# Optimization experiments

Hardware: AMD Instinct MI355X
Metric: run time of the kernel (lower is better)

The kernel has to match this reference:

```python
import jax, jax.numpy as jnp
import numpy as np
from jax.scipy.special import erf

B, S, D, H, F = 2, 2048, 1024, 16, 4096
EPS = 1e-5


def setup_inputs() -> dict:
    key = jax.random.key(0)
    ks = jax.random.split(key, 7)
    s = 0.02  # init scale so attention logits stay in a sane range
    return {
        "x": jax.random.normal(ks[0], (B, S, D), jnp.float32),
        "wq": jax.random.normal(ks[1], (D, D), jnp.float32) * s,
        "wk": jax.random.normal(ks[2], (D, D), jnp.float32) * s,
        "wv": jax.random.normal(ks[3], (D, D), jnp.float32) * s,
        "wo": jax.random.normal(ks[4], (D, D), jnp.float32) * s,
        "w1": jax.random.normal(ks[5], (F, D), jnp.float32) * s,
        "w2": jax.random.normal(ks[6], (D, F), jnp.float32) * s,
        "g1": jnp.ones((D,), jnp.float32),
        "g2": jnp.ones((D,), jnp.float32),
    }


def _rmsnorm(x, g):
    return x / jnp.sqrt(jnp.mean(x * x, axis=-1, keepdims=True) + EPS) * g


def _gelu_exact(x):
    # 0.5 * x * (1 + erf(x / sqrt(2)))
    return 0.5 * x * (1.0 + erf(x * (1.0 / np.sqrt(2.0).astype(np.float32))))


def reference(x, wq, wk, wv, wo, w1, w2, g1, g2):
    b, s, d = x.shape
    dk = d // H
    # --- attention sublayer (pre-RMSNorm) ---
    h = _rmsnorm(x, g1)
    # Linear(bias=False): y = h @ W.T; split heads -> [b, H, s, dk]
    q = (h @ wq.T).reshape(b, s, H, dk).transpose(0, 2, 1, 3)
    k = (h @ wk.T).reshape(b, s, H, dk).transpose(0, 2, 1, 3)
    v = (h @ wv.T).reshape(b, s, H, dk).transpose(0, 2, 1, 3)
    scores = jnp.einsum('bhqd,bhkd->bhqk', q, k) / jnp.sqrt(jnp.float32(dk))
    causal = jnp.triu(jnp.ones((s, s), bool), 1)  # True above diagonal -> masked
    scores = jnp.where(causal, -jnp.inf, scores)
    attn = jax.nn.softmax(scores, axis=-1)
    o = jnp.einsum('bhqk,bhkd->bhqd', attn, v)
    o = o.transpose(0, 2, 1, 3).reshape(b, s, d) @ wo.T
    x = x + o
    # --- FFN sublayer (pre-RMSNorm, exact-erf GELU) ---
    h2 = _rmsnorm(x, g2)
    f = _gelu_exact(h2 @ w1.T) @ w2.T
    return x + f
```

## Files before the change

### kernel.cpp

```cpp
#include <hip/hip_runtime.h>
#include <hip/hip_bf16.h>
#include <math.h>

#define B_   2
#define S_   2048
#define D_   1024
#define H_   16
#define DK_  64
#define F_   4096
#define NTOK (B_ * S_)

typedef __bf16 bf16x8 __attribute__((ext_vector_type(8)));
typedef float  f32x4  __attribute__((ext_vector_type(4)));

__device__ __forceinline__ unsigned short bf16r(float f) {
  unsigned u = __builtin_bit_cast(unsigned, f);
  u += 0x7fffu + ((u >> 16) & 1u);
  return (unsigned short)(u >> 16);
}

__device__ __forceinline__ void gload_lds16(const void* g, void* l) {
  __builtin_amdgcn_global_load_lds(
      (__attribute__((address_space(1))) void*)g,
      (__attribute__((address_space(3))) void*)l, 16, 0, 0);
}

__device__ __forceinline__ unsigned lds_off(void* p) {
  return (unsigned)(size_t)(__attribute__((address_space(3))) void*)p;
}
__device__ __forceinline__ bf16x8 ds_read16(unsigned a) {
  bf16x8 r;
  asm volatile("ds_read_b128 %0, %1" : "=v"(r) : "v"(a));
  return r;
}
__device__ __forceinline__ void ds_write32(unsigned a, unsigned v) {
  asm volatile("ds_write_b32 %0, %1" : : "v"(a), "v"(v));
}
__device__ __forceinline__ void ds_write16b(unsigned a, unsigned v) {
  asm volatile("ds_write_b16 %0, %1" : : "v"(a), "v"(v));
}
__device__ __forceinline__ float fexp2(float x) {
  float r;
  asm volatile("v_exp_f32 %0, %1\n\ts_nop 0" : "=v"(r) : "v"(x));
  return r;
}
__device__ __forceinline__ unsigned cvt_pk_bf16(float lo, float hi) {
  unsigned r;
  asm volatile("v_cvt_pk_bf16_f32 %0, %1, %2" : "=v"(r) : "v"(lo), "v"(hi));
  return r;
}

__device__ __forceinline__ float gelu_fast(float x) {
  float y = 0.7978845608f * x * (1.0f + 0.044715f * x * x);
  float e = fexp2(2.885390082f * y);
  float t = 1.0f - 2.0f / (e + 1.0f);
  return 0.5f * x * (1.0f + t);
}

#define QSCL 0.18033688f

struct CvtArgs {
  const float* src[6];
  unsigned short* dst[6];
  int start[7];
};
__global__ __launch_bounds__(256) void cvt_all_kernel(CvtArgs a) {
  int i = blockIdx.x * blockDim.x + threadIdx.x;
  if (i >= a.start[6]) return;
  int k = 0;
#pragma unroll
  for (int j = 1; j < 6; ++j)
    if (i >= a.start[j]) k = j;
  int off = i - a.start[k];
  float4 v = reinterpret_cast<const float4*>(a.src[k])[off];
  ushort4 o;
  o.x = bf16r(v.x); o.y = bf16r(v.y); o.z = bf16r(v.z); o.w = bf16r(v.w);
  reinterpret_cast<ushort4*>(a.dst[k])[off] = o;
}

__global__ __launch_bounds__(256) void rmsnorm_kernel(
    const float* __restrict__ x, const float* __restrict__ g,
    unsigned short* __restrict__ out) {
  int row = blockIdx.x;
  int t = threadIdx.x, lane = t & 63, w = t >> 6;
  float4 v = reinterpret_cast<const float4*>(x + (size_t)row * D_)[t];
  float ss = v.x * v.x + v.y * v.y + v.z * v.z + v.w * v.w;
#pragma unroll
  for (int d = 1; d < 64; d <<= 1) ss += __shfl_xor(ss, d);
  __shared__ float red[4];
  if (lane == 0) red[w] = ss;
  __syncthreads();
  float tot = red[0] + red[1] + red[2] + red[3];
  float rstd = rsqrtf(tot * (1.0f / D_) + 1e-5f);
  float4 gv = reinterpret_cast<const float4*>(g)[t];
  ushort4 o;
  o.x = bf16r(v.x * rstd * gv.x);
  o.y = bf16r(v.y * rstd * gv.y);
  o.z = bf16r(v.z * rstd * gv.z);
  o.w = bf16r(v.w * rstd * gv.w);
  reinterpret_cast<ushort4*>(out + (size_t)row * D_)[t] = o;
}

__device__ __forceinline__ void store_tile_coalesced(
    const f32x4 (&acc)[4][4], unsigned ew, int lane, int lg, int ln,
    unsigned short* __restrict__ dst, size_t stride, int rowbase, int colbase,
    bool gelu, float scl) {
#pragma unroll
  for (int m = 0; m < 4; ++m)
#pragma unroll
    for (int n = 0; n < 4; ++n)
#pragma unroll
      for (int j = 0; j < 4; ++j) {
        int lrow = lg * 4 + m * 16 + j;
        int lcol = n * 16 + ln;
        int g = (lcol >> 3) ^ (lrow & 7);
        float v = acc[m][n][j];
        if (gelu) v = gelu_fast(v);
        ds_write16b(ew + (unsigned)((lrow * 64 + g * 8 + (lcol & 7)) * 2),
                    (unsigned)bf16r(v * scl));
      }
  asm volatile("s_waitcnt lgkmcnt(0)");
  __builtin_amdgcn_sched_barrier(0);
  bf16x8 cv[8];
#pragma unroll
  for (int i = 0; i < 8; ++i) {
    int lrow = i * 8 + (lane >> 3);
    int g = (lane & 7) ^ (lrow & 7);
    cv[i] = ds_read16(ew + (unsigned)((lrow * 64 + g * 8) * 2));
  }
  asm volatile("s_waitcnt lgkmcnt(0)");
  __builtin_amdgcn_sched_barrier(0);
#pragma unroll
  for (int i = 0; i < 8; ++i) {
    int lrow = i * 8 + (lane >> 3);
    *reinterpret_cast<bf16x8*>(
        &dst[(size_t)(rowbase + lrow) * stride + colbase + (lane & 7) * 8]) = cv[i];
  }
}

__global__ __launch_bounds__(512, 4) void ffn1_gemm(
    const unsigned short* __restrict__ A, const unsigned short* __restrict__ Bw,
    int M, int N, int K, unsigned short* __restrict__ outB) {
  constexpr int BUFU = 12288;
  __shared__ __attribute__((aligned(16))) unsigned short lds[3 * BUFU];
  const int t = threadIdx.x, lane = t & 63, w = t >> 6;
  const int wm = w >> 1, wn = w & 1;
  const int lg = lane >> 4, ln = lane & 15;

  const int gx = gridDim.x;
  int bid = blockIdx.y * gx + blockIdx.x;
  int xcd = bid & 7, c = bid >> 3;
  int RX = gx >> 2, RY = gridDim.y >> 1;
  int bx = (xcd & 3) * RX + (c % RX);
  int by = (xcd >> 2) * RY + (c / RX);
  const int m0 = by * 256, n0 = bx * 128;

  const int nt = K >> 5;

  auto stage = [&](int tile) {
    int buf = tile % 3;
    const int k0 = tile << 5;
    unsigned short* la = &lds[buf * BUFU];
    unsigned short* lb = la + 8192;
#pragma unroll
    for (int i = 0; i < 2; ++i) {
      int g = i * 512 + t;
      int Ln = g >> 3, p = g & 7, u = p ^ (Ln & 7);
      int row = 2 * Ln + (u >> 2), cg = u & 3;
      gload_lds16(A + (size_t)(m0 + row) * K + k0 + cg * 8, &la[g * 8]);
    }
    {
      int Ln = t >> 3, p = t & 7, u = p ^ (Ln & 7);
      int row = 2 * Ln + (u >> 2), cg = u & 3;
      gload_lds16(Bw + (size_t)(n0 + row) * K + k0 + cg * 8, &lb[t * 8]);
    }
  };

  stage(0);
  stage(1);

  const unsigned base0 = lds_off(lds);
  unsigned offA[4], offB[4];
#pragma unroll
  for (int m = 0; m < 4; ++m) {
    int r = wm * 64 + m * 16 + ln;
    int Ln = r >> 1, p = ((r & 1) * 4 + lg) ^ (Ln & 7);
    offA[m] = (unsigned)((Ln * 64 + p * 8) * 2);
  }
#pragma unroll
  for (int n = 0; n < 4; ++n) {
    int r = wn * 64 + n * 16 + ln;
    int Ln = r >> 1, p = ((r & 1) * 4 + lg) ^ (Ln & 7);
    offB[n] = (unsigned)(16384 + (Ln * 64 + p * 8) * 2);
  }

  f32x4 acc[4][4] = {};

  for (int tile = 0; tile < nt; ++tile) {
    if (tile + 1 < nt) { asm volatile("s_waitcnt vmcnt(3)"); }
    else               { asm volatile("s_waitcnt vmcnt(0)"); }
    __builtin_amdgcn_sched_barrier(0);
    __builtin_amdgcn_s_barrier();
    const unsigned bb = base0 + (unsigned)((tile % 3) * (BUFU * 2));
    bf16x8 af[4], bf0, bf1;
#pragma unroll
    for (int m = 0; m < 4; ++m) af[m] = ds_read16(bb + offA[m]);
    bf0 = ds_read16(bb + offB[0]);
    bf1 = ds_read16(bb + offB[1]);
    if (tile + 2 < nt) stage(tile + 2);
    asm volatile("s_waitcnt lgkmcnt(0)");
    __builtin_amdgcn_sched_barrier(0);
    __builtin_amdgcn_s_setprio(1);
#pragma unroll
    for (int m = 0; m < 4; ++m) {
      acc[m][0] = __builtin_amdgcn_mfma_f32_16x16x32_bf16(af[m], bf0, acc[m][0], 0, 0, 0);
      acc[m][1] = __builtin_amdgcn_mfma_f32_16x16x32_bf16(af[m], bf1, acc[m][1], 0, 0, 0);
    }
    __builtin_amdgcn_s_setprio(0);
    bf0 = ds_read16(bb + offB[2]);
    bf1 = ds_read16(bb + offB[3]);
    asm volatile("s_waitcnt lgkmcnt(0)");
    __builtin_amdgcn_sched_barrier(0);
    __builtin_amdgcn_s_setprio(1);
#pragma unroll
    for (int m = 0; m < 4; ++m) {
      acc[m][2] = __builtin_amdgcn_mfma_f32_16x16x32_bf16(af[m], bf0, acc[m][2], 0, 0, 0);
      acc[m][3] = __builtin_amdgcn_mfma_f32_16x16x32_bf16(af[m], bf1, acc[m][3], 0, 0, 0);
    }
    __builtin_amdgcn_s_setprio(0);
  }

  __builtin_amdgcn_s_barrier();
  const unsigned ew = base0 + (unsigned)(w * 8192);
  store_tile_coalesced(acc, ew, lane, lg, ln, outB, (size_t)N,
                       m0 + wm * 64, n0 + wn * 64, true, 1.0f);
}

__global__ __launch_bounds__(256, 2) void qkv_gemm(
    const unsigned short* __restrict__ A, const unsigned short* __restrict__ Bw,
    int M, int N, int K,
    unsigned short* __restrict__ outB, unsigned short* __restrict__ outB2,
    unsigned short* __restrict__ outB3) {
  constexpr int BUFU = 8192;
  __shared__ __attribute__((aligned(16))) unsigned short lds[4 * BUFU];
  const int t = threadIdx.x, lane = t & 63, w = t >> 6;
  const int wm = w >> 1, wn = w & 1;
  const int lg = lane >> 4, ln = lane & 15;

  const int gx = gridDim.x;
  int bid = blockIdx.y * gx + blockIdx.x;
  int xcd = bid & 7, c = bid >> 3;
  int RX = gx >> 2, RY = gridDim.y >> 1;
  int bx = (xcd & 3) * RX + (c % RX);
  int by = (xcd >> 2) * RY + (c / RX);
  const int m0 = by * 128, n0 = bx * 128;

  const int nt = K >> 5;

  auto stage = [&](int tile) {
    int buf = tile & 3;
    const int k0 = tile << 5;
    unsigned short* la = &lds[buf * BUFU];
    unsigned short* lb = la + 4096;
#pragma unroll
    for (int i = 0; i < 2; ++i) {
      int g = i * 256 + t;
      int Ln = g >> 3, p = g & 7, u = p ^ (Ln & 7);
      int row = 2 * Ln + (u >> 2), cg = u & 3;
      gload_lds16(A + (size_t)(m0 + row) * K + k0 + cg * 8, &la[g * 8]);
    }
#pragma unroll
    for (int i = 0; i < 2; ++i) {
      int g = i * 256 + t;
      int Ln = g >> 3, p = g & 7, u = p ^ (Ln & 7);
      int row = 2 * Ln + (u >> 2), cg = u & 3;
      gload_lds16(Bw + (size_t)(n0 + row) * K + k0 + cg * 8, &lb[g * 8]);
    }
  };

  stage(0);
  stage(1);

  const unsigned base0 = lds_off(lds);
  unsigned offA[4], offB[4];
#pragma unroll
  for (int m = 0; m < 4; ++m) {
    int r = wm * 64 + m * 16 + ln;
    int Ln = r >> 1, p = ((r & 1) * 4 + lg) ^ (Ln & 7);
    offA[m] = (unsigned)((Ln * 64 + p * 8) * 2);
  }
#pragma unroll
  for (int n = 0; n < 4; ++n) {
    int r = wn * 64 + n * 16 + ln;
    int Ln = r >> 1, p = ((r & 1) * 4 + lg) ^ (Ln & 7);
    offB[n] = (unsigned)(8192 + (Ln * 64 + p * 8) * 2);
  }

  f32x4 acc[4][4] = {};

  for (int tp = 0; tp < nt; tp += 2) {
    asm volatile("s_waitcnt vmcnt(0)");
    __builtin_amdgcn_sched_barrier(0);
    __builtin_amdgcn_s_barrier();
    const unsigned bb0 = base0 + (unsigned)((tp & 3) * (BUFU * 2));
    const unsigned bb1 = base0 + (unsigned)(((tp + 1) & 3) * (BUFU * 2));
    bf16x8 af[4], bf[4], af2[4], bf2[4];
#pragma unroll
    for (int m = 0; m < 4; ++m) af[m] = ds_read16(bb0 + offA[m]);
#pragma unroll
    for (int n = 0; n < 4; ++n) bf[n] = ds_read16(bb0 + offB[n]);
#pragma unroll
    for (int m = 0; m < 4; ++m) af2[m] = ds_read16(bb1 + offA[m]);
#pragma unroll
    for (int n = 0; n < 4; ++n) bf2[n] = ds_read16(bb1 + offB[n]);
    if (tp + 2 < nt) stage(tp + 2);
    if (tp + 3 < nt) stage(tp + 3);
    asm volatile("s_waitcnt lgkmcnt(8)");
    __builtin_amdgcn_sched_barrier(0);
    __builtin_amdgcn_s_setprio(1);
#pragma unroll
    for (int m = 0; m < 4; ++m)
#pragma unroll
      for (int n = 0; n < 4; ++n)
        acc[m][n] = __builtin_amdgcn_mfma_f32_16x16x32_bf16(af[m], bf[n], acc[m][n], 0, 0, 0);
    __builtin_amdgcn_s_setprio(0);
    asm volatile("s_waitcnt lgkmcnt(0)");
    __builtin_amdgcn_sched_barrier(0);
    __builtin_amdgcn_s_setprio(1);
#pragma unroll
    for (int m = 0; m < 4; ++m)
#pragma unroll
      for (int n = 0; n < 4; ++n)
        acc[m][n] = __builtin_amdgcn_mfma_f32_16x16x32_bf16(af2[m], bf2[n], acc[m][n], 0, 0, 0);
    __builtin_amdgcn_s_setprio(0);
  }

  __builtin_amdgcn_s_barrier();
  const unsigned ew = base0 + (unsigned)(w * 8192);
  const int col0 = n0 + wn * 64;
  const int rowbase = m0 + wm * 64;
  if (col0 < 2 * D_) {
    const float scl = (col0 < D_) ? QSCL : 1.0f;
    unsigned short* dst = (col0 < D_) ? outB : outB2;
    const int cb = (col0 < D_) ? col0 : col0 - D_;
    store_tile_coalesced(acc, ew, lane, lg, ln, dst, (size_t)D_,
                         rowbase, cb, false, scl);
  } else {
    const int cb = col0 - 2 * D_;
    const int bb2 = rowbase >> 11;
    const int s0base = rowbase & (S_ - 1);
#pragma unroll
    for (int m = 0; m < 4; ++m) {
#pragma unroll
      for (int n = 0; n < 4; ++n) {
        int col = cb + n * 16 + ln;
        ushort4 pk;
        pk.x = bf16r(acc[m][n][0]);
        pk.y = bf16r(acc[m][n][1]);
        pk.z = bf16r(acc[m][n][2]);
        pk.w = bf16r(acc[m][n][3]);
        *reinterpret_cast<ushort4*>(
            &outB3[((size_t)(bb2 * D_) + col) * S_ + s0base + lg * 4 + m * 16]) = pk;
      }
    }
  }
}

__device__ __forceinline__ void gemm128_body(
    const unsigned short* __restrict__ A, const unsigned short* __restrict__ Bw,
    int M, int N, int K,
    const float* __restrict__ resid, float* __restrict__ outF) {
  constexpr int BUFU = 256 * 32;
  __shared__ __attribute__((aligned(16))) unsigned short lds[4 * BUFU];
  const int t = threadIdx.x, lane = t & 63, w = t >> 6;
  const int wm = w >> 2, wn = w & 3;
  const int lg = lane >> 4, ln = lane & 15;

  const int gx = gridDim.x;
  int bid = blockIdx.y * gx + blockIdx.x;
  int RX = gx >> 2, RY = gridDim.y >> 1;
  int xcd = bid & 7, c = bid >> 3;
  int bx = (xcd & 3) * RX + (c % RX);
  int by = (xcd >> 2) * RY + (c / RX);
  const int m0 = by * 128, n0 = bx * 128;

  const int nt = K >> 5;

  auto stage = [&](int tile) {
    const int buf = tile & 3;
    const int k0 = tile << 5;
    unsigned short* la = &lds[buf * BUFU];
    unsigned short* lb = la + 4096;
    int Ln = t >> 3, p = t & 7, u = p ^ (Ln & 7);
    int row = 2 * Ln + (u >> 2), cg = u & 3;
    gload_lds16(A + (size_t)(m0 + row) * K + k0 + cg * 8, &la[t * 8]);
    gload_lds16(Bw + (size_t)(n0 + row) * K + k0 + cg * 8, &lb[t * 8]);
  };

  stage(0);
  if (nt > 1) stage(1);
  if (nt > 2) stage(2);

  const unsigned base0 = lds_off(lds);
  unsigned offA[4], offB[2];
#pragma unroll
  for (int m = 0; m < 4; ++m) {
    int r = wm * 64 + m * 16 + ln;
    int Ln = r >> 1, p = ((r & 1) * 4 + lg) ^ (Ln & 7);
    offA[m] = (unsigned)((Ln * 64 + p * 8) * 2);
  }
#pragma unroll
  for (int n = 0; n < 2; ++n) {
    int r = wn * 32 + n * 16 + ln;
    int Ln = r >> 1, p = ((r & 1) * 4 + lg) ^ (Ln & 7);
    offB[n] = (unsigned)(8192 + (Ln * 64 + p * 8) * 2);
  }

  f32x4 acc[4][2] = {};

  for (int tile = 0; tile < nt; ++tile) {
    const int rem = nt - 1 - tile;
    if (rem >= 2)      { asm volatile("s_waitcnt vmcnt(4)"); }
    else if (rem == 1) { asm volatile("s_waitcnt vmcnt(2)"); }
    else               { asm volatile("s_waitcnt vmcnt(0)"); }
    __builtin_amdgcn_sched_barrier(0);
    __builtin_amdgcn_s_barrier();
    const unsigned bb = base0 + (unsigned)((tile & 3) * (BUFU * 2));
    bf16x8 af[4], bf[2];
#pragma unroll
    for (int m = 0; m < 4; ++m) af[m] = ds_read16(bb + offA[m]);
#pragma unroll
    for (int n = 0; n < 2; ++n) bf[n] = ds_read16(bb + offB[n]);
    if (tile + 3 < nt) stage(tile + 3);
    asm volatile("s_waitcnt lgkmcnt(0)");
    __builtin_amdgcn_sched_barrier(0);
    __builtin_amdgcn_s_setprio(1);
#pragma unroll
    for (int m = 0; m < 4; ++m)
#pragma unroll
      for (int n = 0; n < 2; ++n)
        acc[m][n] = __builtin_amdgcn_mfma_f32_16x16x32_bf16(af[m], bf[n], acc[m][n], 0, 0, 0);
    __builtin_amdgcn_s_setprio(0);
  }

  const int rbase = m0 + wm * 64 + lg * 4;
  const int cbase = n0 + wn * 32 + ln;
#pragma unroll
  for (int m = 0; m < 4; ++m) {
#pragma unroll
    for (int n = 0; n < 2; ++n) {
      int col = cbase + n * 16;
#pragma unroll
      for (int j = 0; j < 4; ++j) {
        int row = rbase + m * 16 + j;
        outF[(size_t)row * N + col] = acc[m][n][j] + resid[(size_t)row * N + col];
      }
    }
  }
}

__global__ __launch_bounds__(512, 4) void wo_gemm(
    const unsigned short* __restrict__ A, const unsigned short* __restrict__ Bw,
    int M, int N, int K, const float* __restrict__ resid, float* __restrict__ outF) {
  gemm128_body(A, Bw, M, N, K, resid, outF);
}
__global__ __launch_bounds__(512, 4) void ffn2_gemm(
    const unsigned short* __restrict__ A, const unsigned short* __restrict__ Bw,
    int M, int N, int K, const float* __restrict__ resid, float* __restrict__ outF) {
  gemm128_body(A, Bw, M, N, K, resid, outF);
}

#define PV_ISSUE(c, pa, v0, v1, v2, v3) do {                                   \
  unsigned cg_ = (unsigned)(((((c) * 4) + lg) ^ ln) & 15);                     \
  pa = ds_read16(pbase + (unsigned)(ln * 256) + cg_ * 16);                     \
  v0 = ds_read16(vb + (unsigned)((0 * 16 + ln) * 256) + cg_ * 16);             \
  v1 = ds_read16(vb + (unsigned)((1 * 16 + ln) * 256) + cg_ * 16);             \
  v2 = ds_read16(vb + (unsigned)((2 * 16 + ln) * 256) + cg_ * 16);             \
  v3 = ds_read16(vb + (unsigned)((3 * 16 + ln) * 256) + cg_ * 16);             \
} while (0)

#define PV_MFMA(pa, v0, v1, v2, v3) do {                                       \
  oacc[0] = __builtin_amdgcn_mfma_f32_16x16x32_bf16(pa, v0, oacc[0], 0, 0, 0); \
  oacc[1] = __builtin_amdgcn_mfma_f32_16x16x32_bf16(pa, v1, oacc[1], 0, 0, 0); \
  oacc[2] = __builtin_amdgcn_mfma_f32_16x16x32_bf16(pa, v2, oacc[2], 0, 0, 0); \
  oacc[3] = __builtin_amdgcn_mfma_f32_16x16x32_bf16(pa, v3, oacc[3], 0, 0, 0); \
} while (0)

__global__ __launch_bounds__(256, 2) void attn_kernel(
    const unsigned short* __restrict__ qg, const unsigned short* __restrict__ kg,
    const unsigned short* __restrict__ vt, unsigned short* __restrict__ og) {
  __shared__ __attribute__((aligned(16))) unsigned short Kl[2][8192];
  __shared__ __attribute__((aligned(16))) unsigned short Vl[2][8192];
  __shared__ __attribute__((aligned(16))) unsigned short Pl[4][2048];
  const int t = threadIdx.x, lane = t & 63, w = t >> 6;
  const int lg = lane >> 4, ln = lane & 15;

  int bid = blockIdx.x;
  int nl = (bid & 7) * 64 + (bid >> 3);
  int bh = nl >> 4, pi = nl & 15;
  int b = bh >> 4, h = bh & 15;

  const unsigned kbase = lds_off(&Kl[0][0]);
  const unsigned vbase = lds_off(&Vl[0][0]);
  const unsigned pbase = lds_off(&Pl[w][0]);

  auto runq = [&](int qtile, bool first) {
    const int q0 = qtile * 64;
    const int qw = q0 + w * 16;
    const int nt = (q0 >> 7) + 1;

    bf16x8 aq[2];
    {
      const unsigned short* qp =
          qg + (size_t)(b * S_ + qw + ln) * D_ + h * DK_ + lg * 8;
      aq[0] = *reinterpret_cast<const bf16x8*>(qp);
      aq[1] = *reinterpret_cast<const bf16x8*>(qp + 32);
    }
    asm volatile("" : : "v"(aq[0]), "v"(aq[1]));

    float mr = -1e30f, lr = 0.f;
    f32x4 oacc[4] = {};

    auto stage = [&](int kt) {
      const int buf = kt & 1;
      const int kv0 = kt * 128;
#pragma unroll
      for (int i = 0; i < 4; ++i) {
        int g = i * 256 + t;
        int row = g >> 3, cg = g & 7, sg = cg ^ (row & 7);
        gload_lds16(kg + (size_t)(b * S_ + kv0 + row) * D_ + h * DK_ + sg * 8,
                    &Kl[buf][g * 8]);
      }
#pragma unroll
      for (int i = 0; i < 4; ++i) {
        int g = i * 256 + t;
        int row = g >> 4, cg = g & 15, sg = cg ^ (row & 15);
        gload_lds16(vt + (size_t)(b * D_ + h * DK_ + row) * S_ + kv0 + sg * 8,
                    &Vl[buf][g * 8]);
      }
    };

    if (!first) __builtin_amdgcn_s_barrier();
    stage(0);

    auto ctile = [&](int kt, bool dm) {
      const unsigned kb = kbase + (unsigned)((kt & 1) * 16384);
      const unsigned vb = vbase + (unsigned)((kt & 1) * 16384);
      f32x4 sc[8] = {};
      bf16x8 kf[8], kf2[8];
#pragma unroll
      for (int n = 0; n < 8; ++n) {
        int r = n * 16 + ln;
        int cg0 = lg ^ (r & 7);
        kf[n] = ds_read16(kb + (unsigned)((r * 128 + cg0 * 16)));
      }
#pragma unroll
      for (int n = 0; n < 8; ++n) {
        int r = n * 16 + ln;
        int cg1 = (4 + lg) ^ (r & 7);
        kf2[n] = ds_read16(kb + (unsigned)((r * 128 + cg1 * 16)));
      }
      if (!dm) stage(kt + 1);
      asm volatile("s_waitcnt lgkmcnt(8)");
      __builtin_amdgcn_sched_barrier(0);
#pragma unroll
      for (int n = 0; n < 8; ++n)
        sc[n] = __builtin_amdgcn_mfma_f32_16x16x32_bf16(kf[n], aq[0], sc[n], 0, 0, 0);
      asm volatile("s_waitcnt lgkmcnt(0)");
      __builtin_amdgcn_sched_barrier(0);
#pragma unroll
      for (int n = 0; n < 8; ++n)
        sc[n] = __builtin_amdgcn_mfma_f32_16x16x32_bf16(kf2[n], aq[1], sc[n], 0, 0, 0);
      if (dm) {
        const int kv0 = kt * 128;
        const int qi = qw + ln;
#pragma unroll
        for (int n = 0; n < 8; ++n)
#pragma unroll
          for (int j = 0; j < 4; ++j)
            if ((kv0 + n * 16 + lg * 4 + j) > qi) sc[n][j] = -1e30f;
      }
      float mx = -1e30f;
#pragma unroll
      for (int n = 0; n < 8; ++n) {
        float a = fmaxf(fmaxf(sc[n][0], sc[n][1]), fmaxf(sc[n][2], sc[n][3]));
        mx = fmaxf(mx, a);
      }
      mx = fmaxf(mx, __shfl_xor(mx, 16));
      mx = fmaxf(mx, __shfl_xor(mx, 32));
      float mn = fmaxf(mr, mx);
      float ps = 0.f;
#pragma unroll
      for (int n = 0; n < 8; ++n)
#pragma unroll
        for (int j = 0; j < 4; ++j) {
          float p = fexp2(sc[n][j] - mn);
          sc[n][j] = p;
          ps += p;
        }
      if (__all(mx <= mr)) {
        lr += ps;
      } else {
        float sf = fexp2(mr - mn);
        mr = mn;
        lr = lr * sf + ps;
#pragma unroll
        for (int j = 0; j < 4; ++j) {
          float sfj = __shfl(sf, lg * 4 + j);
#pragma unroll
          for (int f = 0; f < 4; ++f) oacc[f][j] *= sfj;
        }
      }
#pragma unroll
      for (int n = 0; n < 8; ++n) {
        int kvc = n * 16 + lg * 4;
        int gsw = ((kvc >> 3) ^ ln) & 15;
        unsigned pa_addr = pbase + (unsigned)(ln * 256 + gsw * 16 + (kvc & 7) * 2);
        ds_write32(pa_addr, cvt_pk_bf16(sc[n][0], sc[n][1]));
        ds_write32(pa_addr + 4, cvt_pk_bf16(sc[n][2], sc[n][3]));
      }
      asm volatile("s_waitcnt lgkmcnt(0)");
      __builtin_amdgcn_sched_barrier(0);
      bf16x8 paA, vA0, vA1, vA2, vA3, paB, vB0, vB1, vB2, vB3;
      PV_ISSUE(0, paA, vA0, vA1, vA2, vA3);
      PV_ISSUE(1, paB, vB0, vB1, vB2, vB3);
      asm volatile("s_waitcnt lgkmcnt(5)");
      __builtin_amdgcn_sched_barrier(0);
      PV_MFMA(paA, vA0, vA1, vA2, vA3);
      PV_ISSUE(2, paA, vA0, vA1, vA2, vA3);
      asm volatile("s_waitcnt lgkmcnt(5)");
      __builtin_amdgcn_sched_barrier(0);
      PV_MFMA(paB, vB0, vB1, vB2, vB3);
      PV_ISSUE(3, paB, vB0, vB1, vB2, vB3);
      asm volatile("s_waitcnt lgkmcnt(5)");
      __builtin_amdgcn_sched_barrier(0);
      PV_MFMA(paA, vA0, vA1, vA2, vA3);
      asm volatile("s_waitcnt lgkmcnt(0)");
      __builtin_amdgcn_sched_barrier(0);
      PV_MFMA(paB, vB0, vB1, vB2, vB3);
    };

    for (int kt = 0; kt < nt - 1; ++kt) {
      asm volatile("s_waitcnt vmcnt(0)");
      __builtin_amdgcn_sched_barrier(0);
      __builtin_amdgcn_s_barrier();
      ctile(kt, false);
    }
    asm volatile("s_waitcnt vmcnt(0)");
    __builtin_amdgcn_sched_barrier(0);
    __builtin_amdgcn_s_barrier();
    ctile(nt - 1, true);

    lr += __shfl_xor(lr, 16);
    lr += __shfl_xor(lr, 32);
#pragma unroll
    for (int j = 0; j < 4; ++j) {
      float lj = __shfl(lr, lg * 4 + j);
      float inv = 1.0f / lj;
      int row = b * S_ + qw + lg * 4 + j;
#pragma unroll
      for (int f = 0; f < 4; ++f)
        og[(size_t)row * D_ + h * DK_ + f * 16 + ln] = bf16r(oacc[f][j] * inv);
    }
  };

  runq(31 - pi, true);
  runq(pi, false);
}

extern "C" void kernel_launch(void* const* d_in, const int* in_sizes, int n_in,
                              void* d_out, int out_size, void* d_ws, size_t ws_size,
                              hipStream_t stream) {
  const float* x  = (const float*)d_in[0];
  const float* wq = (const float*)d_in[1];
  const float* wk = (const float*)d_in[2];
  const float* wv = (const float*)d_in[3];
  const float* wo = (const float*)d_in[4];
  const float* w1 = (const float*)d_in[5];
  const float* w2 = (const float*)d_in[6];
  const float* g1 = (const float*)d_in[7];
  const float* g2 = (const float*)d_in[8];
  float* out = (float*)d_out;

  char* ws = (char*)d_ws;
  const size_t MB = 1024 * 1024;
  unsigned short* wqkv_b = (unsigned short*)(ws + 0 * MB);
  unsigned short* wo_b   = (unsigned short*)(ws + 6 * MB);
  unsigned short* w1_b   = (unsigned short*)(ws + 8 * MB);
  unsigned short* w2_b   = (unsigned short*)(ws + 16 * MB);
  unsigned short* h_b    = (unsigned short*)(ws + 24 * MB);
  unsigned short* q_b    = (unsigned short*)(ws + 32 * MB);
  unsigned short* k_b    = (unsigned short*)(ws + 40 * MB);
  unsigned short* vt_b   = (unsigned short*)(ws + 48 * MB);
  unsigned short* o_b    = (unsigned short*)(ws + 56 * MB);
  float*          x1     = (float*)(ws + 64 * MB);
  unsigned short* mid    = (unsigned short*)(ws + 80 * MB);

  CvtArgs ca;
  ca.src[0] = wq; ca.dst[0] = wqkv_b;
  ca.src[1] = wk; ca.dst[1] = wqkv_b + (size_t)D_ * D_;
  ca.src[2] = wv; ca.dst[2] = wqkv_b + (size_t)2 * D_ * D_;
  ca.src[3] = wo; ca.dst[3] = wo_b;
  ca.src[4] = w1; ca.dst[4] = w1_b;
  ca.src[5] = w2; ca.dst[5] = w2_b;
  int q4 = D_ * D_ / 4, f4 = F_ * D_ / 4;
  ca.start[0] = 0;
  ca.start[1] = q4;
  ca.start[2] = 2 * q4;
  ca.start[3] = 3 * q4;
  ca.start[4] = 4 * q4;
  ca.start[5] = 4 * q4 + f4;
  ca.start[6] = 4 * q4 + 2 * f4;
  cvt_all_kernel<<<(ca.start[6] + 255) / 256, 256, 0, stream>>>(ca);

  rmsnorm_kernel<<<NTOK, 256, 0, stream>>>(x, g1, h_b);

  qkv_gemm<<<dim3(3 * D_ / 128, NTOK / 128), dim3(256), 0, stream>>>(
      h_b, wqkv_b, NTOK, 3 * D_, D_, q_b, k_b, vt_b);

  attn_kernel<<<dim3(512), dim3(256), 0, stream>>>(q_b, k_b, vt_b, o_b);

  wo_gemm<<<dim3(D_ / 128, NTOK / 128), dim3(512), 0, stream>>>(
      o_b, wo_b, NTOK, D_, D_, x, x1);

  rmsnorm_kernel<<<NTOK, 256, 0, stream>>>(x1, g2, h_b);

  ffn1_gemm<<<dim3(F_ / 128, NTOK / 256), dim3(512), 0, stream>>>(
      h_b, w1_b, NTOK, F_, D_, mid);

  ffn2_gemm<<<dim3(D_ / 128, NTOK / 128), dim3(512), 0, stream>>>(
      mid, w2_b, NTOK, D_, F_, x1, out);
}
```

Before: 206.2 us.

## Enlarge FFN1 GEMM tile to 256x256 with K=64 double-buffered pipeline

The FFN1 GEMM now uses a 256x256 output tile per block instead of 256x128. Each of its 8 waves owns a 128x64 sub-tile, and K steps advance by 64 with two LDS buffers of 64 KB each in total. Global-to-LDS loads for the next tile are interleaved across four MFMA quarter-phases with barriers between them. This is meant to raise arithmetic intensity and cut global/LDS traffic per FLOP. The cost is higher register pressure (32 accumulators per wave), lower occupancy (launch bounds drop from 4 to 2), more barriers, and half as many blocks in the grid.

```diff
diff --git a/kernel.cpp b/kernel.cpp
--- a/kernel.cpp
+++ b/kernel.cpp
@@ -138,13 +138,12 @@
   }
 }
 
-__global__ __launch_bounds__(512, 4) void ffn1_gemm(
+__global__ __launch_bounds__(512, 2) void ffn1_gemm(
     const unsigned short* __restrict__ A, const unsigned short* __restrict__ Bw,
     int M, int N, int K, unsigned short* __restrict__ outB) {
-  constexpr int BUFU = 12288;
-  __shared__ __attribute__((aligned(16))) unsigned short lds[3 * BUFU];
+  __shared__ __attribute__((aligned(16))) unsigned short lds[65536];
   const int t = threadIdx.x, lane = t & 63, w = t >> 6;
-  const int wm = w >> 1, wn = w & 1;
+  const int wm = w >> 2, wn = w & 3;
   const int lg = lane >> 4, ln = lane & 15;
 
   const int gx = gridDim.x;
@@ -153,87 +152,152 @@
   int RX = gx >> 2, RY = gridDim.y >> 1;
   int bx = (xcd & 3) * RX + (c % RX);
   int by = (xcd >> 2) * RY + (c / RX);
-  const int m0 = by * 256, n0 = bx * 128;
-
-  const int nt = K >> 5;
-
-  auto stage = [&](int tile) {
-    int buf = tile % 3;
-    const int k0 = tile << 5;
-    unsigned short* la = &lds[buf * BUFU];
-    unsigned short* lb = la + 8192;
+  const int m0 = by * 256, n0 = bx * 256;
+
+  const int nt = K >> 6;
+  const int niter = nt >> 1;
+
+  auto SA = [&](int tile, int h) {
+    unsigned short* dst = &lds[(tile & 1) * 32768 + h * 8192];
+    const int k0 = tile << 6;
+    const int rb = m0 + h * 128;
 #pragma unroll
     for (int i = 0; i < 2; ++i) {
       int g = i * 512 + t;
-      int Ln = g >> 3, p = g & 7, u = p ^ (Ln & 7);
-      int row = 2 * Ln + (u >> 2), cg = u & 3;
-      gload_lds16(A + (size_t)(m0 + row) * K + k0 + cg * 8, &la[g * 8]);
-    }
-    {
-      int Ln = t >> 3, p = t & 7, u = p ^ (Ln & 7);
-      int row = 2 * Ln + (u >> 2), cg = u & 3;
-      gload_lds16(Bw + (size_t)(n0 + row) * K + k0 + cg * 8, &lb[t * 8]);
+      int row = g >> 3, sg = (g & 7) ^ (row & 7);
+      gload_lds16(A + (size_t)(rb + row) * K + k0 + sg * 8, &dst[g * 8]);
     }
   };
-
-  stage(0);
-  stage(1);
+  auto SB = [&](int tile, int h) {
+    unsigned short* dst = &lds[(tile & 1) * 32768 + 16384 + h * 8192];
+    const int k0 = tile << 6;
+    const int rb = n0 + h * 128;
+#pragma unroll
+    for (int i = 0; i < 2; ++i) {
+      int g = i * 512 + t;
+      int row = g >> 3, sg = (g & 7) ^ (row & 7);
+      gload_lds16(Bw + (size_t)(rb + row) * K + k0 + sg * 8, &dst[g * 8]);
+    }
+  };
+
+  SA(0, 0); SA(0, 1); SB(0, 0); SB(0, 1); SB(1, 0); SB(1, 1);
 
   const unsigned base0 = lds_off(lds);
-  unsigned offA[4], offB[4];
-#pragma unroll
-  for (int m = 0; m < 4; ++m) {
-    int r = wm * 64 + m * 16 + ln;
-    int Ln = r >> 1, p = ((r & 1) * 4 + lg) ^ (Ln & 7);
-    offA[m] = (unsigned)((Ln * 64 + p * 8) * 2);
+  unsigned offA[8], offB[4];
+#pragma unroll
+  for (int m = 0; m < 8; ++m) {
+    int r = wm * 128 + m * 16 + ln;
+    offA[m] = (unsigned)(r * 128 + (lg ^ (r & 7)) * 16);
   }
 #pragma unroll
   for (int n = 0; n < 4; ++n) {
     int r = wn * 64 + n * 16 + ln;
-    int Ln = r >> 1, p = ((r & 1) * 4 + lg) ^ (Ln & 7);
-    offB[n] = (unsigned)(16384 + (Ln * 64 + p * 8) * 2);
-  }
-
-  f32x4 acc[4][4] = {};
-
-  for (int tile = 0; tile < nt; ++tile) {
-    if (tile + 1 < nt) { asm volatile("s_waitcnt vmcnt(3)"); }
-    else               { asm volatile("s_waitcnt vmcnt(0)"); }
-    __builtin_amdgcn_sched_barrier(0);
-    __builtin_amdgcn_s_barrier();
-    const unsigned bb = base0 + (unsigned)((tile % 3) * (BUFU * 2));
-    bf16x8 af[4], bf0, bf1;
-#pragma unroll
-    for (int m = 0; m < 4; ++m) af[m] = ds_read16(bb + offA[m]);
-    bf0 = ds_read16(bb + offB[0]);
-    bf1 = ds_read16(bb + offB[1]);
-    if (tile + 2 < nt) stage(tile + 2);
-    asm volatile("s_waitcnt lgkmcnt(0)");
-    __builtin_amdgcn_sched_barrier(0);
-    __builtin_amdgcn_s_setprio(1);
-#pragma unroll
-    for (int m = 0; m < 4; ++m) {
-      acc[m][0] = __builtin_amdgcn_mfma_f32_16x16x32_bf16(af[m], bf0, acc[m][0], 0, 0, 0);
-      acc[m][1] = __builtin_amdgcn_mfma_f32_16x16x32_bf16(af[m], bf1, acc[m][1], 0, 0, 0);
-    }
-    __builtin_amdgcn_s_setprio(0);
-    bf0 = ds_read16(bb + offB[2]);
-    bf1 = ds_read16(bb + offB[3]);
-    asm volatile("s_waitcnt lgkmcnt(0)");
-    __builtin_amdgcn_sched_barrier(0);
-    __builtin_amdgcn_s_setprio(1);
-#pragma unroll
-    for (int m = 0; m < 4; ++m) {
-      acc[m][2] = __builtin_amdgcn_mfma_f32_16x16x32_bf16(af[m], bf0, acc[m][2], 0, 0, 0);
-      acc[m][3] = __builtin_amdgcn_mfma_f32_16x16x32_bf16(af[m], bf1, acc[m][3], 0, 0, 0);
-    }
-    __builtin_amdgcn_s_setprio(0);
-  }
-
+    offB[n] = (unsigned)(32768 + r * 128 + (lg ^ (r & 7)) * 16);
+  }
+
+  f32x4 acc[8][4] = {};
+
+  asm volatile("s_waitcnt vmcnt(0)");
+  __builtin_amdgcn_sched_barrier(0);
   __builtin_amdgcn_s_barrier();
+
+  for (int it = 0; it < niter; ++it) {
+    const int t0 = 2 * it, t1 = 2 * it + 1;
+    const bool more = (it + 1 < niter);
+    const unsigned bb0 = base0 + (unsigned)((t0 & 1) * 65536);
+    const unsigned bb1 = base0 + (unsigned)((t1 & 1) * 65536);
+    bf16x8 bfr[4][2];
+#pragma unroll
+    for (int q = 0; q < 4; ++q) {
+      bf16x8 af[2][2];
+      if (q == 0) {
+#pragma unroll
+        for (int n = 0; n < 4; ++n) {
+          bfr[n][0] = ds_read16(bb0 + offB[n]);
+          bfr[n][1] = ds_read16(bb0 + (offB[n] ^ 0x40u));
+        }
+      }
+#pragma unroll
+      for (int mm = 0; mm < 2; ++mm) {
+        af[mm][0] = ds_read16(bb0 + offA[2 * q + mm]);
+        af[mm][1] = ds_read16(bb0 + (offA[2 * q + mm] ^ 0x40u));
+      }
+      if (q == 0)       SA(t1, 0);
+      else if (q == 1)  SA(t1, 1);
+      else if (q == 2)  { if (more) SB(t0 + 2, 0); }
+      else              { if (more) SB(t0 + 2, 1); }
+      if (q == 3) {
+        if (more) { asm volatile("s_waitcnt vmcnt(4)"); }
+        else      { asm volatile("s_waitcnt vmcnt(0)"); }
+        __builtin_amdgcn_sched_barrier(0);
+      }
+      __builtin_amdgcn_s_barrier();
+      asm volatile("s_waitcnt lgkmcnt(0)");
+      __builtin_amdgcn_sched_barrier(0);
+      __builtin_amdgcn_s_setprio(1);
+#pragma unroll
+      for (int mm = 0; mm < 2; ++mm)
+#pragma unroll
+        for (int n = 0; n < 4; ++n) {
+          acc[2 * q + mm][n] = __builtin_amdgcn_mfma_f32_16x16x32_bf16(
+              af[mm][0], bfr[n][0], acc[2 * q + mm][n], 0, 0, 0);
+          acc[2 * q + mm][n] = __builtin_amdgcn_mfma_f32_16x16x32_bf16(
+              af[mm][1], bfr[n][1], acc[2 * q + mm][n], 0, 0, 0);
+        }
+      __builtin_amdgcn_s_setprio(0);
+      __builtin_amdgcn_s_barrier();
+    }
+#pragma unroll
+    for (int q = 0; q < 4; ++q) {
+      bf16x8 af[2][2];
+      if (q == 0) {
+#pragma unroll
+        for (int n = 0; n < 4; ++n) {
+          bfr[n][0] = ds_read16(bb1 + offB[n]);
+          bfr[n][1] = ds_read16(bb1 + (offB[n] ^ 0x40u));
+        }
+      }
+#pragma unroll
+      for (int mm = 0; mm < 2; ++mm) {
+        af[mm][0] = ds_read16(bb1 + offA[2 * q + mm]);
+        af[mm][1] = ds_read16(bb1 + (offA[2 * q + mm] ^ 0x40u));
+      }
+      if (more) {
+        if (q == 0)      SA(t0 + 2, 0);
+        else if (q == 1) SA(t0 + 2, 1);
+        else if (q == 2) SB(t1 + 2, 0);
+        else             SB(t1 + 2, 1);
+      }
+      if (q == 3) {
+        if (more) { asm volatile("s_waitcnt vmcnt(4)"); }
+        else      { asm volatile("s_waitcnt vmcnt(0)"); }
+        __builtin_amdgcn_sched_barrier(0);
+      }
+      __builtin_amdgcn_s_barrier();
+      asm volatile("s_waitcnt lgkmcnt(0)");
+      __builtin_amdgcn_sched_barrier(0);
+      __builtin_amdgcn_s_setprio(1);
+#pragma unroll
+      for (int mm = 0; mm < 2; ++mm)
+#pragma unroll
+        for (int n = 0; n < 4; ++n) {
+          acc[2 * q + mm][n] = __builtin_amdgcn_mfma_f32_16x16x32_bf16(
+              af[mm][0], bfr[n][0], acc[2 * q + mm][n], 0, 0, 0);
+          acc[2 * q + mm][n] = __builtin_amdgcn_mfma_f32_16x16x32_bf16(
+              af[mm][1], bfr[n][1], acc[2 * q + mm][n], 0, 0, 0);
+        }
+      __builtin_amdgcn_s_setprio(0);
+      __builtin_amdgcn_s_barrier();
+    }
+  }
+
   const unsigned ew = base0 + (unsigned)(w * 8192);
-  store_tile_coalesced(acc, ew, lane, lg, ln, outB, (size_t)N,
-                       m0 + wm * 64, n0 + wn * 64, true, 1.0f);
+  store_tile_coalesced(*reinterpret_cast<const f32x4(*)[4][4]>(&acc[0]),
+                       ew, lane, lg, ln, outB, (size_t)N,
+                       m0 + wm * 128, n0 + wn * 64, true, 1.0f);
+  store_tile_coalesced(*reinterpret_cast<const f32x4(*)[4][4]>(&acc[4]),
+                       ew, lane, lg, ln, outB, (size_t)N,
+                       m0 + wm * 128 + 64, n0 + wn * 64, true, 1.0f);
 }
 
 __global__ __launch_bounds__(256, 2) void qkv_gemm(
@@ -725,7 +789,7 @@
 
   rmsnorm_kernel<<<NTOK, 256, 0, stream>>>(x1, g2, h_b);
 
-  ffn1_gemm<<<dim3(F_ / 128, NTOK / 256), dim3(512), 0, stream>>>(
+  ffn1_gemm<<<dim3(F_ / 256, NTOK / 256), dim3(512), 0, stream>>>(
       h_b, w1_b, NTOK, F_, D_, mid);
 
   ffn2_gemm<<<dim3(D_ / 128, NTOK / 128), dim3(512), 0, stream>>>(
```

Result: no change. 202.4 us, median of 2 (-1.9%).
